# Optimization experiments

Hardware: AMD Instinct MI355X
Metric: run time of the kernel (lower is better)

The kernel has to match this reference:

```python
import jax, jax.numpy as jnp
import numpy as np

N = 100_000      # n_nodes
DEG = 32         # edge_threshold (fixed out-degree)
D = 64           # in_channels = out_channels, heads = 1
NEG_SLOPE = 0.2


def setup_inputs() -> dict:
    key = jax.random.key(0)
    k1, k2, k3, k4 = jax.random.split(key, 4)
    x = jax.random.normal(k1, (N, D), jnp.float32)
    # fixed-degree edge list with no self loops (offset in [1, N-1])
    src = jnp.repeat(jnp.arange(N, dtype=jnp.int64), DEG)
    off = jax.random.randint(k2, (N * DEG,), 1, N, dtype=jnp.int64)
    dst = (src + off) % N
    edge_index = jnp.stack([src, dst])  # [2, E]
    # glorot init as in the torch module
    stdv_w = float(np.sqrt(6.0 / (D + D)))
    weight = jax.random.uniform(k3, (D, D), jnp.float32, -stdv_w, stdv_w)
    stdv_a = float(np.sqrt(6.0 / (1 + 2 * D)))  # att is [1, heads=1, 2*D]
    att = jax.random.uniform(k4, (2 * D,), jnp.float32, -stdv_a, stdv_a)
    bias = jnp.zeros((D,), jnp.float32)
    return {"x": x, "edge_index": edge_index, "weight": weight, "att": att, "bias": bias}


def reference(x, edge_index, weight, att, bias):
    n, d = x.shape
    h = x @ weight                               # [N, D] (heads=1)
    # add self loops (inputs are constructed without self loops)
    loop = jnp.arange(n, dtype=edge_index.dtype)
    src = jnp.concatenate([edge_index[0], loop])  # message sources (x_j)
    dst = jnp.concatenate([edge_index[1], loop])  # aggregation targets (x_i)
    # GAT edge score: (cat([x_i, x_j]) * att).sum(-1) = h_i@a_i + h_j@a_j
    a_i, a_j = att[:d], att[d:]
    s_i = h @ a_i                                 # [N]
    s_j = h @ a_j                                 # [N]
    alpha = s_i[dst] + s_j[src]                   # [E+N]
    alpha = jnp.where(alpha > 0, alpha, NEG_SLOPE * alpha)  # leaky_relu
    # segment softmax over destination nodes (numerically stable)
    amax = jax.ops.segment_max(alpha, dst, num_segments=n)
    e = jnp.exp(alpha - amax[dst])
    denom = jax.ops.segment_sum(e, dst, num_segments=n)
    w = e / (denom[dst] + 1e-16)                  # [E+N]
    # weighted scatter-add aggregation of source features
    out = jax.ops.segment_sum(h[src] * w[:, None], dst, num_segments=n)  # [N, D]
    out = out + bias                              # head-mean is identity (heads=1)
    # dropout(p=0.5) is identity in eval mode; F.normalize (L2, dim=1, eps=1e-12)
    norm = jnp.linalg.norm(out, axis=1, keepdims=True)
    return out / jnp.maximum(norm, 1e-12)
```

## Files before the change

kernel.cpp:

```cpp
#include <hip/hip_runtime.h>
#include <math.h>

#define NEG_SLOPE 0.2f
#define PCHUNK 4096
#define NBINS_MAX 392
#define BIN_EDGE_CAP 8704

__device__ __forceinline__ unsigned pk_bf16x2(float a, float b) {
    unsigned ua = __float_as_uint(a);
    ua = (ua + 0x7FFFu + ((ua >> 16) & 1u)) >> 16;
    unsigned ub = __float_as_uint(b);
    ub = (ub + 0x7FFFu + ((ub >> 16) & 1u)) & 0xFFFF0000u;
    return ua | ub;
}

__global__ __launch_bounds__(256) void k_linear(const float* __restrict__ x,
        const float* __restrict__ W, const float* __restrict__ att,
        uint2* __restrict__ h16, float* __restrict__ si, float* __restrict__ sj,
        int n)
{
    int tid = threadIdx.x;
    int lane = tid & 63;
    int wv = tid >> 6;
    int q = lane >> 4;
    int f = lane & 15;

    const float4* W4 = (const float4*)W;
    float4 Wr[16];
#pragma unroll
    for (int kb = 0; kb < 16; ++kb)
        Wr[kb] = W4[(16 * q + kb) * 16 + f];

    const float4* att4 = (const float4*)att;
    float4 ai4 = att4[f];
    float4 aj4 = att4[16 + f];
    const float4* x4 = (const float4*)x;

    int row0 = (blockIdx.x * 4 + wv) * 8;
    for (int r = 0; r < 8; ++r) {
        int row = row0 + r;
        if (row >= n) break;
        size_t xb = (size_t)row * 16 + 4 * q;
        float4 xq0 = x4[xb + 0];
        float4 xq1 = x4[xb + 1];
        float4 xq2 = x4[xb + 2];
        float4 xq3 = x4[xb + 3];
        float4 acc = {0.f, 0.f, 0.f, 0.f};
#define LSTEP(xc, kb) { float4 w4 = Wr[kb]; \
        acc.x = fmaf((xc), w4.x, acc.x); acc.y = fmaf((xc), w4.y, acc.y); \
        acc.z = fmaf((xc), w4.z, acc.z); acc.w = fmaf((xc), w4.w, acc.w); }
        LSTEP(xq0.x, 0)  LSTEP(xq0.y, 1)  LSTEP(xq0.z, 2)  LSTEP(xq0.w, 3)
        LSTEP(xq1.x, 4)  LSTEP(xq1.y, 5)  LSTEP(xq1.z, 6)  LSTEP(xq1.w, 7)
        LSTEP(xq2.x, 8)  LSTEP(xq2.y, 9)  LSTEP(xq2.z, 10) LSTEP(xq2.w, 11)
        LSTEP(xq3.x, 12) LSTEP(xq3.y, 13) LSTEP(xq3.z, 14) LSTEP(xq3.w, 15)
#undef LSTEP
        acc.x += __shfl_xor(acc.x, 16); acc.x += __shfl_xor(acc.x, 32);
        acc.y += __shfl_xor(acc.y, 16); acc.y += __shfl_xor(acc.y, 32);
        acc.z += __shfl_xor(acc.z, 16); acc.z += __shfl_xor(acc.z, 32);
        acc.w += __shfl_xor(acc.w, 16); acc.w += __shfl_xor(acc.w, 32);

        if (q == 0) {
            uint2 p;
            p.x = pk_bf16x2(acc.x, acc.y);
            p.y = pk_bf16x2(acc.z, acc.w);
            h16[(size_t)row * 16 + f] = p;
        }

        float p = acc.x * ai4.x + acc.y * ai4.y + acc.z * ai4.z + acc.w * ai4.w;
        float pq = acc.x * aj4.x + acc.y * aj4.y + acc.z * aj4.z + acc.w * aj4.w;
#pragma unroll
        for (int o = 8; o >= 1; o >>= 1) {
            p += __shfl_xor(p, o);
            pq += __shfl_xor(pq, o);
        }
        if (lane == 0) { si[row] = p; sj[row] = pq; }
    }
}

__global__ __launch_bounds__(256) void k_hist(const int* __restrict__ dst, int E,
        int* __restrict__ hist_g, int NB, int nbins)
{
    __shared__ int hist[NBINS_MAX];
    int tid = threadIdx.x;
    int blk = blockIdx.x;
    int base = blk * PCHUNK;
    int cnt = E - base;
    if (cnt > PCHUNK) cnt = PCHUNK;
    for (int b = tid; b < nbins; b += 256) hist[b] = 0;
    __syncthreads();
    for (int i = tid; i < cnt; i += 256)
        atomicAdd(&hist[dst[base + i] >> 8], 1);
    __syncthreads();
    for (int b = tid; b < nbins; b += 256)
        hist_g[(size_t)b * NB + blk] = hist[b];
}

__global__ __launch_bounds__(256) void k_scan_a(int* __restrict__ data,
        int* __restrict__ bsum, int M)
{
    __shared__ int wsum[4];
    int tid = threadIdx.x;
    int lane = tid & 63;
    int wv = tid >> 6;
    int i0 = blockIdx.x * 1024 + tid * 4;
    int d0 = 0, d1 = 0, d2 = 0, d3 = 0;
    if (i0 + 3 < M) {
        int4 v = *(const int4*)(data + i0);
        d0 = v.x; d1 = v.y; d2 = v.z; d3 = v.w;
    } else {
        if (i0 + 0 < M) d0 = data[i0 + 0];
        if (i0 + 1 < M) d1 = data[i0 + 1];
        if (i0 + 2 < M) d2 = data[i0 + 2];
        if (i0 + 3 < M) d3 = data[i0 + 3];
    }
    int s = d0 + d1 + d2 + d3;
    int v = s;
#pragma unroll
    for (int o = 1; o < 64; o <<= 1) {
        int t = __shfl_up(v, o);
        if (lane >= o) v += t;
    }
    if (lane == 63) wsum[wv] = v;
    __syncthreads();
    int woff = 0;
    for (int w = 0; w < wv; ++w) woff += wsum[w];
    int ex = v - s + woff;
    if (i0 + 0 < M) data[i0 + 0] = ex; ex += d0;
    if (i0 + 1 < M) data[i0 + 1] = ex; ex += d1;
    if (i0 + 2 < M) data[i0 + 2] = ex; ex += d2;
    if (i0 + 3 < M) data[i0 + 3] = ex;
    if (tid == 255) bsum[blockIdx.x] = wsum[0] + wsum[1] + wsum[2] + wsum[3];
}

__global__ __launch_bounds__(256) void k_scan_b(const int* __restrict__ bsum,
        int* __restrict__ boff, int nb)
{
    __shared__ int wsum[4];
    int tid = threadIdx.x;
    int lane = tid & 63;
    int wv = tid >> 6;
    int t2 = tid * 2;
    int a = (t2 < nb) ? bsum[t2] : 0;
    int b = (t2 + 1 < nb) ? bsum[t2 + 1] : 0;
    int s = a + b;
    int v = s;
#pragma unroll
    for (int o = 1; o < 64; o <<= 1) {
        int t = __shfl_up(v, o);
        if (lane >= o) v += t;
    }
    if (lane == 63) wsum[wv] = v;
    __syncthreads();
    int woff = 0;
    for (int w = 0; w < wv; ++w) woff += wsum[w];
    int ex = v - s + woff;
    if (t2 < nb) boff[t2] = ex;
    if (t2 + 1 < nb) boff[t2 + 1] = ex + a;
}

__global__ __launch_bounds__(256) void k_scan_c(int* __restrict__ data,
        const int* __restrict__ boff, int M)
{
    int off = boff[blockIdx.x];
    int i0 = blockIdx.x * 1024 + threadIdx.x * 4;
#pragma unroll
    for (int k = 0; k < 4; ++k)
        if (i0 + k < M) data[i0 + k] += off;
}

__global__ __launch_bounds__(256) void k_part2(const int* __restrict__ src,
        const int* __restrict__ dst, int E,
        const int* __restrict__ hist_g, int NB, int nbins,
        unsigned* __restrict__ bin_edges)
{
    __shared__ unsigned stage[PCHUNK];
    __shared__ unsigned short sbin[PCHUNK];
    __shared__ int hist[NBINS_MAX];
    __shared__ int off[NBINS_MAX + 1];
    __shared__ int cur[NBINS_MAX];
    __shared__ int gbase[NBINS_MAX];
    __shared__ int wsum[4];

    int tid = threadIdx.x;
    int blk = blockIdx.x;
    int base = blk * PCHUNK;
    int cnt = E - base;
    if (cnt > PCHUNK) cnt = PCHUNK;

    for (int b = tid; b < nbins; b += 256) hist[b] = 0;
    __syncthreads();
    for (int i = tid; i < cnt; i += 256)
        atomicAdd(&hist[dst[base + i] >> 8], 1);
    __syncthreads();

    int lane = tid & 63;
    int wv = tid >> 6;
    int t2 = tid * 2;
    int a = (t2 < nbins) ? hist[t2] : 0;
    int b2 = (t2 + 1 < nbins) ? hist[t2 + 1] : 0;
    int s = a + b2;
    int v = s;
#pragma unroll
    for (int o = 1; o < 64; o <<= 1) {
        int t = __shfl_up(v, o);
        if (lane >= o) v += t;
    }
    if (lane == 63) wsum[wv] = v;
    __syncthreads();
    int woff = 0;
    for (int w = 0; w < wv; ++w) woff += wsum[w];
    int ex = v - s + woff;
    if (t2 <= nbins) off[t2] = ex;
    if (t2 + 1 <= nbins) off[t2 + 1] = ex + a;
    __syncthreads();

    for (int b = tid; b < nbins; b += 256) {
        cur[b] = off[b];
        gbase[b] = hist_g[(size_t)b * NB + blk];
    }
    __syncthreads();

    for (int i = tid; i < cnt; i += 256) {
        int e = base + i;
        int d = dst[e];
        int bb = d >> 8;
        int pos = atomicAdd(&cur[bb], 1);
        stage[pos] = ((unsigned)(d & 255) << 17) | (unsigned)src[e];
        sbin[pos] = (unsigned short)bb;
    }
    __syncthreads();
    for (int i = tid; i < cnt; i += 256) {
        int bb = sbin[i];
        bin_edges[gbase[bb] + (i - off[bb])] = stage[i];
    }
}

__global__ __launch_bounds__(256) void k_csr(const int* __restrict__ hist_g,
        int NB, int E, unsigned* __restrict__ bin_edges,
        int* __restrict__ row_start, int* __restrict__ deg, int n)
{
    __shared__ unsigned stage[BIN_EDGE_CAP];
    __shared__ int cnt256[256];
    __shared__ int off256[256];
    __shared__ int wsum[4];
    int b = blockIdx.x;
    int tid = threadIdx.x;
    int base = hist_g[(size_t)b * NB];
    int nxt = (b + 1 < (int)gridDim.x) ? hist_g[(size_t)(b + 1) * NB] : E;
    int cntE = nxt - base;
    if (cntE > BIN_EDGE_CAP) cntE = BIN_EDGE_CAP;

    for (int i = tid; i < cntE; i += 256) stage[i] = bin_edges[base + i];
    cnt256[tid] = 0;
    __syncthreads();
    for (int i = tid; i < cntE; i += 256)
        atomicAdd(&cnt256[stage[i] >> 17], 1);
    __syncthreads();

    int lane = tid & 63;
    int wv = tid >> 6;
    int s = cnt256[tid];
    int v = s;
#pragma unroll
    for (int o = 1; o < 64; o <<= 1) {
        int t = __shfl_up(v, o);
        if (lane >= o) v += t;
    }
    if (lane == 63) wsum[wv] = v;
    __syncthreads();
    int woff = 0;
    for (int w = 0; w < wv; ++w) woff += wsum[w];
    int ex = v - s + woff;
    off256[tid] = ex;

    int gd = b * 256 + tid;
    if (gd < n) {
        row_start[gd] = base + ex;
        deg[gd] = s;
    }
    __syncthreads();
    cnt256[tid] = ex;
    __syncthreads();
    for (int i = tid; i < cntE; i += 256) {
        unsigned pk = stage[i];
        int dl = (int)(pk >> 17);
        int pos = atomicAdd(&cnt256[dl], 1);
        bin_edges[base + pos] = pk & 0x1FFFFu;
    }
}

__global__ __launch_bounds__(256) void k_agg(const uint2* __restrict__ h16,
        const float* __restrict__ si, const float* __restrict__ sj,
        const int* __restrict__ row_start, const int* __restrict__ deg_arr,
        const unsigned* __restrict__ cols,
        const float* __restrict__ bias, float* __restrict__ out, int n)
{
    __shared__ int   sArr[4][132];
    __shared__ float wArr[4][132];
    int lane = threadIdx.x & 63;
    int wv = threadIdx.x >> 6;
    int d = blockIdx.x * 4 + wv;
    if (d >= n) return;

    int dg = deg_arr[d];
    if (dg > 128) dg = 128;
    int rs = row_start[d];
    float sid = si[d];

    int s0 = 0, s1 = 0;
    float a0 = -1e30f, a1 = -1e30f;
    if (lane < dg) {
        s0 = (int)cols[rs + lane];
        float t = sid + sj[s0];
        a0 = t > 0.f ? t : NEG_SLOPE * t;
    }
    if (lane + 64 < dg) {
        s1 = (int)cols[rs + lane + 64];
        float t = sid + sj[s1];
        a1 = t > 0.f ? t : NEG_SLOPE * t;
    }
    float tself = sid + sj[d];
    float aself = tself > 0.f ? tself : NEG_SLOPE * tself;

    float m = fmaxf(fmaxf(a0, a1), aself);
#pragma unroll
    for (int o = 32; o >= 1; o >>= 1) m = fmaxf(m, __shfl_xor(m, o));

    float e0 = (lane < dg) ? __expf(a0 - m) : 0.f;
    float e1 = (lane + 64 < dg) ? __expf(a1 - m) : 0.f;
    float eself = __expf(aself - m);

    float dsum = e0 + e1;
#pragma unroll
    for (int o = 32; o >= 1; o >>= 1) dsum += __shfl_xor(dsum, o);
    dsum += eself;

    if (lane < dg) { sArr[wv][lane] = s0; wArr[wv][lane] = e0; }
    if (lane + 64 < dg) { sArr[wv][lane + 64] = s1; wArr[wv][lane + 64] = e1; }
    if (lane == 0) { sArr[wv][dg] = d; wArr[wv][dg] = eself; }
    int cntAll = dg + 1;

    int q = lane >> 4;
    int f = lane & 15;
    float4 acc0 = {0.f, 0.f, 0.f, 0.f};
    float4 acc1 = {0.f, 0.f, 0.f, 0.f};
    int j = q;
    for (; j + 4 < cntAll; j += 8) {
        int   sA = sArr[wv][j];     float wA = wArr[wv][j];
        int   sB = sArr[wv][j + 4]; float wB = wArr[wv][j + 4];
        uint2 hA = h16[(size_t)sA * 16 + f];
        uint2 hB = h16[(size_t)sB * 16 + f];
        float ax = __uint_as_float(hA.x << 16);
        float ay = __uint_as_float(hA.x & 0xFFFF0000u);
        float az = __uint_as_float(hA.y << 16);
        float aw = __uint_as_float(hA.y & 0xFFFF0000u);
        float bx = __uint_as_float(hB.x << 16);
        float by = __uint_as_float(hB.x & 0xFFFF0000u);
        float bz = __uint_as_float(hB.y << 16);
        float bw = __uint_as_float(hB.y & 0xFFFF0000u);
        acc0.x = fmaf(wA, ax, acc0.x); acc0.y = fmaf(wA, ay, acc0.y);
        acc0.z = fmaf(wA, az, acc0.z); acc0.w = fmaf(wA, aw, acc0.w);
        acc1.x = fmaf(wB, bx, acc1.x); acc1.y = fmaf(wB, by, acc1.y);
        acc1.z = fmaf(wB, bz, acc1.z); acc1.w = fmaf(wB, bw, acc1.w);
    }
    if (j < cntAll) {
        int sA = sArr[wv][j]; float wA = wArr[wv][j];
        uint2 hA = h16[(size_t)sA * 16 + f];
        float ax = __uint_as_float(hA.x << 16);
        float ay = __uint_as_float(hA.x & 0xFFFF0000u);
        float az = __uint_as_float(hA.y << 16);
        float aw = __uint_as_float(hA.y & 0xFFFF0000u);
        acc0.x = fmaf(wA, ax, acc0.x); acc0.y = fmaf(wA, ay, acc0.y);
        acc0.z = fmaf(wA, az, acc0.z); acc0.w = fmaf(wA, aw, acc0.w);
    }
    acc0.x += acc1.x; acc0.y += acc1.y; acc0.z += acc1.z; acc0.w += acc1.w;

    acc0.x += __shfl_xor(acc0.x, 16); acc0.x += __shfl_xor(acc0.x, 32);
    acc0.y += __shfl_xor(acc0.y, 16); acc0.y += __shfl_xor(acc0.y, 32);
    acc0.z += __shfl_xor(acc0.z, 16); acc0.z += __shfl_xor(acc0.z, 32);
    acc0.w += __shfl_xor(acc0.w, 16); acc0.w += __shfl_xor(acc0.w, 32);

    float inv = 1.f / (dsum + 1e-16f);
    const float4* b4 = (const float4*)bias;
    float4 bb = b4[f];
    float4 o4;
    o4.x = acc0.x * inv + bb.x;
    o4.y = acc0.y * inv + bb.y;
    o4.z = acc0.z * inv + bb.z;
    o4.w = acc0.w * inv + bb.w;

    float nsq = o4.x * o4.x + o4.y * o4.y + o4.z * o4.z + o4.w * o4.w;
#pragma unroll
    for (int o = 8; o >= 1; o >>= 1) nsq += __shfl_xor(nsq, o);
    float rn = 1.f / fmaxf(sqrtf(nsq), 1e-12f);

    if (q == 0) {
        float4 res;
        res.x = o4.x * rn; res.y = o4.y * rn; res.z = o4.z * rn; res.w = o4.w * rn;
        ((float4*)out)[(size_t)d * 16 + f] = res;
    }
}

extern "C" void kernel_launch(void* const* d_in, const int* in_sizes, int n_in,
                              void* d_out, int out_size, void* d_ws, size_t ws_size,
                              hipStream_t stream)
{
    const float* x    = (const float*)d_in[0];
    const int*   ei   = (const int*)d_in[1];
    const float* W    = (const float*)d_in[2];
    const float* att  = (const float*)d_in[3];
    const float* bias = (const float*)d_in[4];
    float* out = (float*)d_out;

    int n = in_sizes[0] / 64;
    int E = in_sizes[1] / 2;
    const int* src = ei;
    const int* dst = ei + E;

    int nbins = (n + 255) >> 8;
    int NB = (E + PCHUNK - 1) / PCHUNK;
    int M = nbins * NB;
    int nsc = (M + 1023) / 1024;

    char* ws = (char*)d_ws;
#define CARVE(ptr, type, count) type* ptr = (type*)ws; \
        ws += (((size_t)(count) * sizeof(type)) + 255) & ~(size_t)255;
    CARVE(h16, uint2, (size_t)n * 16)
    CARVE(si, float, n)
    CARVE(sj, float, n)
    CARVE(row_start, int, n)
    CARVE(deg, int, n)
    CARVE(hist_g, int, M)
    CARVE(bsum, int, 512)
    CARVE(boff, int, 512)
    CARVE(bin_edges, unsigned, E)
#undef CARVE

    k_linear<<<(n + 31) / 32, 256, 0, stream>>>(x, W, att, h16, si, sj, n);
    k_hist<<<NB, 256, 0, stream>>>(dst, E, hist_g, NB, nbins);
    k_scan_a<<<nsc, 256, 0, stream>>>(hist_g, bsum, M);
    k_scan_b<<<1, 256, 0, stream>>>(bsum, boff, nsc);
    k_scan_c<<<nsc, 256, 0, stream>>>(hist_g, boff, M);
    k_part2<<<NB, 256, 0, stream>>>(src, dst, E, hist_g, NB, nbins, bin_edges);
    k_csr<<<nbins, 256, 0, stream>>>(hist_g, NB, E, bin_edges, row_start, deg, n);
    k_agg<<<(n + 3) / 4, 256, 0, stream>>>(h16, si, sj, row_start, deg, bin_edges, bias, out, n);
}
```

Measured before the change: 263.9 us.

## Replace binned two-pass CSR build with global atomic degree count and scatter

```diff
diff --git a/kernel.cpp b/kernel.cpp
--- a/kernel.cpp
+++ b/kernel.cpp
@@ -2,9 +2,6 @@
 #include <math.h>
 
 #define NEG_SLOPE 0.2f
-#define PCHUNK 4096
-#define NBINS_MAX 392
-#define BIN_EDGE_CAP 8704
 
 __device__ __forceinline__ unsigned pk_bf16x2(float a, float b) {
     unsigned ua = __float_as_uint(a);
@@ -17,9 +14,12 @@
 __global__ __launch_bounds__(256) void k_linear(const float* __restrict__ x,
         const float* __restrict__ W, const float* __restrict__ att,
         uint2* __restrict__ h16, float* __restrict__ si, float* __restrict__ sj,
-        int n)
+        int* __restrict__ deg, int n)
 {
     int tid = threadIdx.x;
+    int g = blockIdx.x * 256 + tid;
+    if (g < n) deg[g] = 0;
+
     int lane = tid & 63;
     int wv = tid >> 6;
     int q = lane >> 4;
@@ -77,26 +77,24 @@
     }
 }
 
-__global__ __launch_bounds__(256) void k_hist(const int* __restrict__ dst, int E,
-        int* __restrict__ hist_g, int NB, int nbins)
-{
-    __shared__ int hist[NBINS_MAX];
-    int tid = threadIdx.x;
-    int blk = blockIdx.x;
-    int base = blk * PCHUNK;
-    int cnt = E - base;
-    if (cnt > PCHUNK) cnt = PCHUNK;
-    for (int b = tid; b < nbins; b += 256) hist[b] = 0;
-    __syncthreads();
-    for (int i = tid; i < cnt; i += 256)
-        atomicAdd(&hist[dst[base + i] >> 8], 1);
-    __syncthreads();
-    for (int b = tid; b < nbins; b += 256)
-        hist_g[(size_t)b * NB + blk] = hist[b];
-}
-
-__global__ __launch_bounds__(256) void k_scan_a(int* __restrict__ data,
-        int* __restrict__ bsum, int M)
+__global__ __launch_bounds__(256) void k_deg(const int* __restrict__ dst, int E,
+        int* __restrict__ deg)
+{
+    int i = (blockIdx.x * 256 + threadIdx.x) * 4;
+    if (i + 3 < E) {
+        int4 v = *(const int4*)(dst + i);
+        atomicAdd(&deg[v.x], 1);
+        atomicAdd(&deg[v.y], 1);
+        atomicAdd(&deg[v.z], 1);
+        atomicAdd(&deg[v.w], 1);
+    } else {
+        for (int k = 0; k < 4; ++k)
+            if (i + k < E) atomicAdd(&deg[dst[i + k]], 1);
+    }
+}
+
+__global__ __launch_bounds__(256) void k_scan_a(const int* __restrict__ in,
+        int* __restrict__ out, int* __restrict__ bsum, int M)
 {
     __shared__ int wsum[4];
     int tid = threadIdx.x;
@@ -105,13 +103,13 @@
     int i0 = blockIdx.x * 1024 + tid * 4;
     int d0 = 0, d1 = 0, d2 = 0, d3 = 0;
     if (i0 + 3 < M) {
-        int4 v = *(const int4*)(data + i0);
+        int4 v = *(const int4*)(in + i0);
         d0 = v.x; d1 = v.y; d2 = v.z; d3 = v.w;
     } else {
-        if (i0 + 0 < M) d0 = data[i0 + 0];
-        if (i0 + 1 < M) d1 = data[i0 + 1];
-        if (i0 + 2 < M) d2 = data[i0 + 2];
-        if (i0 + 3 < M) d3 = data[i0 + 3];
+        if (i0 + 0 < M) d0 = in[i0 + 0];
+        if (i0 + 1 < M) d1 = in[i0 + 1];
+        if (i0 + 2 < M) d2 = in[i0 + 2];
+        if (i0 + 3 < M) d3 = in[i0 + 3];
     }
     int s = d0 + d1 + d2 + d3;
     int v = s;
@@ -125,10 +123,10 @@
     int woff = 0;
     for (int w = 0; w < wv; ++w) woff += wsum[w];
     int ex = v - s + woff;
-    if (i0 + 0 < M) data[i0 + 0] = ex; ex += d0;
-    if (i0 + 1 < M) data[i0 + 1] = ex; ex += d1;
-    if (i0 + 2 < M) data[i0 + 2] = ex; ex += d2;
-    if (i0 + 3 < M) data[i0 + 3] = ex;
+    if (i0 + 0 < M) out[i0 + 0] = ex; ex += d0;
+    if (i0 + 1 < M) out[i0 + 1] = ex; ex += d1;
+    if (i0 + 2 < M) out[i0 + 2] = ex; ex += d2;
+    if (i0 + 3 < M) out[i0 + 3] = ex;
     if (tid == 255) bsum[blockIdx.x] = wsum[0] + wsum[1] + wsum[2] + wsum[3];
 }
 
@@ -158,145 +156,52 @@
     if (t2 + 1 < nb) boff[t2 + 1] = ex + a;
 }
 
-__global__ __launch_bounds__(256) void k_scan_c(int* __restrict__ data,
-        const int* __restrict__ boff, int M)
+__global__ __launch_bounds__(256) void k_scan_c(int* __restrict__ row_start,
+        int* __restrict__ cur, const int* __restrict__ boff, int M)
 {
     int off = boff[blockIdx.x];
     int i0 = blockIdx.x * 1024 + threadIdx.x * 4;
 #pragma unroll
     for (int k = 0; k < 4; ++k)
-        if (i0 + k < M) data[i0 + k] += off;
-}
-
-__global__ __launch_bounds__(256) void k_part2(const int* __restrict__ src,
+        if (i0 + k < M) {
+            int v = row_start[i0 + k] + off;
+            row_start[i0 + k] = v;
+            cur[i0 + k] = v;
+        }
+}
+
+__global__ __launch_bounds__(256) void k_scatter(const int* __restrict__ src,
         const int* __restrict__ dst, int E,
-        const int* __restrict__ hist_g, int NB, int nbins,
-        unsigned* __restrict__ bin_edges)
-{
-    __shared__ unsigned stage[PCHUNK];
-    __shared__ unsigned short sbin[PCHUNK];
-    __shared__ int hist[NBINS_MAX];
-    __shared__ int off[NBINS_MAX + 1];
-    __shared__ int cur[NBINS_MAX];
-    __shared__ int gbase[NBINS_MAX];
-    __shared__ int wsum[4];
-
-    int tid = threadIdx.x;
-    int blk = blockIdx.x;
-    int base = blk * PCHUNK;
-    int cnt = E - base;
-    if (cnt > PCHUNK) cnt = PCHUNK;
-
-    for (int b = tid; b < nbins; b += 256) hist[b] = 0;
-    __syncthreads();
-    for (int i = tid; i < cnt; i += 256)
-        atomicAdd(&hist[dst[base + i] >> 8], 1);
-    __syncthreads();
-
-    int lane = tid & 63;
-    int wv = tid >> 6;
-    int t2 = tid * 2;
-    int a = (t2 < nbins) ? hist[t2] : 0;
-    int b2 = (t2 + 1 < nbins) ? hist[t2 + 1] : 0;
-    int s = a + b2;
-    int v = s;
-#pragma unroll
-    for (int o = 1; o < 64; o <<= 1) {
-        int t = __shfl_up(v, o);
-        if (lane >= o) v += t;
-    }
-    if (lane == 63) wsum[wv] = v;
-    __syncthreads();
-    int woff = 0;
-    for (int w = 0; w < wv; ++w) woff += wsum[w];
-    int ex = v - s + woff;
-    if (t2 <= nbins) off[t2] = ex;
-    if (t2 + 1 <= nbins) off[t2 + 1] = ex + a;
-    __syncthreads();
-
-    for (int b = tid; b < nbins; b += 256) {
-        cur[b] = off[b];
-        gbase[b] = hist_g[(size_t)b * NB + blk];
-    }
-    __syncthreads();
-
-    for (int i = tid; i < cnt; i += 256) {
-        int e = base + i;
-        int d = dst[e];
-        int bb = d >> 8;
-        int pos = atomicAdd(&cur[bb], 1);
-        stage[pos] = ((unsigned)(d & 255) << 17) | (unsigned)src[e];
-        sbin[pos] = (unsigned short)bb;
-    }
-    __syncthreads();
-    for (int i = tid; i < cnt; i += 256) {
-        int bb = sbin[i];
-        bin_edges[gbase[bb] + (i - off[bb])] = stage[i];
-    }
-}
-
-__global__ __launch_bounds__(256) void k_csr(const int* __restrict__ hist_g,
-        int NB, int E, unsigned* __restrict__ bin_edges,
-        int* __restrict__ row_start, int* __restrict__ deg, int n)
-{
-    __shared__ unsigned stage[BIN_EDGE_CAP];
-    __shared__ int cnt256[256];
-    __shared__ int off256[256];
-    __shared__ int wsum[4];
-    int b = blockIdx.x;
-    int tid = threadIdx.x;
-    int base = hist_g[(size_t)b * NB];
-    int nxt = (b + 1 < (int)gridDim.x) ? hist_g[(size_t)(b + 1) * NB] : E;
-    int cntE = nxt - base;
-    if (cntE > BIN_EDGE_CAP) cntE = BIN_EDGE_CAP;
-
-    for (int i = tid; i < cntE; i += 256) stage[i] = bin_edges[base + i];
-    cnt256[tid] = 0;
-    __syncthreads();
-    for (int i = tid; i < cntE; i += 256)
-        atomicAdd(&cnt256[stage[i] >> 17], 1);
-    __syncthreads();
-
-    int lane = tid & 63;
-    int wv = tid >> 6;
-    int s = cnt256[tid];
-    int v = s;
-#pragma unroll
-    for (int o = 1; o < 64; o <<= 1) {
-        int t = __shfl_up(v, o);
-        if (lane >= o) v += t;
-    }
-    if (lane == 63) wsum[wv] = v;
-    __syncthreads();
-    int woff = 0;
-    for (int w = 0; w < wv; ++w) woff += wsum[w];
-    int ex = v - s + woff;
-    off256[tid] = ex;
-
-    int gd = b * 256 + tid;
-    if (gd < n) {
-        row_start[gd] = base + ex;
-        deg[gd] = s;
-    }
-    __syncthreads();
-    cnt256[tid] = ex;
-    __syncthreads();
-    for (int i = tid; i < cntE; i += 256) {
-        unsigned pk = stage[i];
-        int dl = (int)(pk >> 17);
-        int pos = atomicAdd(&cnt256[dl], 1);
-        bin_edges[base + pos] = pk & 0x1FFFFu;
+        int* __restrict__ cur, int* __restrict__ cols)
+{
+    int i = (blockIdx.x * 256 + threadIdx.x) * 4;
+    if (i + 3 < E) {
+        int4 d = *(const int4*)(dst + i);
+        int4 s = *(const int4*)(src + i);
+        int p0 = atomicAdd(&cur[d.x], 1);
+        int p1 = atomicAdd(&cur[d.y], 1);
+        int p2 = atomicAdd(&cur[d.z], 1);
+        int p3 = atomicAdd(&cur[d.w], 1);
+        cols[p0] = s.x;
+        cols[p1] = s.y;
+        cols[p2] = s.z;
+        cols[p3] = s.w;
+    } else {
+        for (int k = 0; k < 4; ++k)
+            if (i + k < E) {
+                int p = atomicAdd(&cur[dst[i + k]], 1);
+                cols[p] = src[i + k];
+            }
     }
 }
 
 __global__ __launch_bounds__(256) void k_agg(const uint2* __restrict__ h16,
         const float* __restrict__ si, const float* __restrict__ sj,
         const int* __restrict__ row_start, const int* __restrict__ deg_arr,
-        const unsigned* __restrict__ cols,
+        const int* __restrict__ cols,
         const float* __restrict__ bias, float* __restrict__ out, int n)
 {
-    __shared__ int   sArr[4][132];
-    __shared__ float wArr[4][132];
+    __shared__ int2 swArr[4][132];
     int lane = threadIdx.x & 63;
     int wv = threadIdx.x >> 6;
     int d = blockIdx.x * 4 + wv;
@@ -310,12 +215,12 @@
     int s0 = 0, s1 = 0;
     float a0 = -1e30f, a1 = -1e30f;
     if (lane < dg) {
-        s0 = (int)cols[rs + lane];
+        s0 = cols[rs + lane];
         float t = sid + sj[s0];
         a0 = t > 0.f ? t : NEG_SLOPE * t;
     }
     if (lane + 64 < dg) {
-        s1 = (int)cols[rs + lane + 64];
+        s1 = cols[rs + lane + 64];
         float t = sid + sj[s1];
         a1 = t > 0.f ? t : NEG_SLOPE * t;
     }
@@ -335,45 +240,64 @@
     for (int o = 32; o >= 1; o >>= 1) dsum += __shfl_xor(dsum, o);
     dsum += eself;
 
-    if (lane < dg) { sArr[wv][lane] = s0; wArr[wv][lane] = e0; }
-    if (lane + 64 < dg) { sArr[wv][lane + 64] = s1; wArr[wv][lane + 64] = e1; }
-    if (lane == 0) { sArr[wv][dg] = d; wArr[wv][dg] = eself; }
+    if (lane < dg) swArr[wv][lane] = make_int2(s0, __float_as_int(e0));
+    if (lane + 64 < dg) swArr[wv][lane + 64] = make_int2(s1, __float_as_int(e1));
+    if (lane == 0) swArr[wv][dg] = make_int2(d, __float_as_int(eself));
     int cntAll = dg + 1;
 
     int q = lane >> 4;
     int f = lane & 15;
     float4 acc0 = {0.f, 0.f, 0.f, 0.f};
     float4 acc1 = {0.f, 0.f, 0.f, 0.f};
+    float4 acc2 = {0.f, 0.f, 0.f, 0.f};
+    float4 acc3 = {0.f, 0.f, 0.f, 0.f};
+
+#define UNPK_FMA(hv, wgt, acc) { \
+        acc.x = fmaf((wgt), __uint_as_float((hv).x << 16), acc.x); \
+        acc.y = fmaf((wgt), __uint_as_float((hv).x & 0xFFFF0000u), acc.y); \
+        acc.z = fmaf((wgt), __uint_as_float((hv).y << 16), acc.z); \
+        acc.w = fmaf((wgt), __uint_as_float((hv).y & 0xFFFF0000u), acc.w); }
+
     int j = q;
+    for (; j + 12 < cntAll; j += 16) {
+        int2 eA = swArr[wv][j];
+        int2 eB = swArr[wv][j + 4];
+        int2 eC = swArr[wv][j + 8];
+        int2 eD = swArr[wv][j + 12];
+        uint2 hA = h16[(size_t)eA.x * 16 + f];
+        uint2 hB = h16[(size_t)eB.x * 16 + f];
+        uint2 hC = h16[(size_t)eC.x * 16 + f];
+        uint2 hD = h16[(size_t)eD.x * 16 + f];
+        float wA = __int_as_float(eA.y);
+        float wB = __int_as_float(eB.y);
+        float wC = __int_as_float(eC.y);
+        float wD = __int_as_float(eD.y);
+        UNPK_FMA(hA, wA, acc0)
+        UNPK_FMA(hB, wB, acc1)
+        UNPK_FMA(hC, wC, acc2)
+        UNPK_FMA(hD, wD, acc3)
+    }
     for (; j + 4 < cntAll; j += 8) {
-        int   sA = sArr[wv][j];     float wA = wArr[wv][j];
-        int   sB = sArr[wv][j + 4]; float wB = wArr[wv][j + 4];
-        uint2 hA = h16[(size_t)sA * 16 + f];
-        uint2 hB = h16[(size_t)sB * 16 + f];
-        float ax = __uint_as_float(hA.x << 16);
-        float ay = __uint_as_float(hA.x & 0xFFFF0000u);
-        float az = __uint_as_float(hA.y << 16);
-        float aw = __uint_as_float(hA.y & 0xFFFF0000u);
-        float bx = __uint_as_float(hB.x << 16);
-        float by = __uint_as_float(hB.x & 0xFFFF0000u);
-        float bz = __uint_as_float(hB.y << 16);
-        float bw = __uint_as_float(hB.y & 0xFFFF0000u);
-        acc0.x = fmaf(wA, ax, acc0.x); acc0.y = fmaf(wA, ay, acc0.y);
-        acc0.z = fmaf(wA, az, acc0.z); acc0.w = fmaf(wA, aw, acc0.w);
-        acc1.x = fmaf(wB, bx, acc1.x); acc1.y = fmaf(wB, by, acc1.y);
-        acc1.z = fmaf(wB, bz, acc1.z); acc1.w = fmaf(wB, bw, acc1.w);
+        int2 eA = swArr[wv][j];
+        int2 eB = swArr[wv][j + 4];
+        uint2 hA = h16[(size_t)eA.x * 16 + f];
+        uint2 hB = h16[(size_t)eB.x * 16 + f];
+        float wA = __int_as_float(eA.y);
+        float wB = __int_as_float(eB.y);
+        UNPK_FMA(hA, wA, acc0)
+        UNPK_FMA(hB, wB, acc1)
     }
     if (j < cntAll) {
-        int sA = sArr[wv][j]; float wA = wArr[wv][j];
-        uint2 hA = h16[(size_t)sA * 16 + f];
-        float ax = __uint_as_float(hA.x << 16);
-        float ay = __uint_as_float(hA.x & 0xFFFF0000u);
-        float az = __uint_as_float(hA.y << 16);
-        float aw = __uint_as_float(hA.y & 0xFFFF0000u);
-        acc0.x = fmaf(wA, ax, acc0.x); acc0.y = fmaf(wA, ay, acc0.y);
-        acc0.z = fmaf(wA, az, acc0.z); acc0.w = fmaf(wA, aw, acc0.w);
-    }
+        int2 eA = swArr[wv][j];
+        uint2 hA = h16[(size_t)eA.x * 16 + f];
+        float wA = __int_as_float(eA.y);
+        UNPK_FMA(hA, wA, acc0)
+    }
+#undef UNPK_FMA
+
     acc0.x += acc1.x; acc0.y += acc1.y; acc0.z += acc1.z; acc0.w += acc1.w;
+    acc2.x += acc3.x; acc2.y += acc3.y; acc2.z += acc3.z; acc2.w += acc3.w;
+    acc0.x += acc2.x; acc0.y += acc2.y; acc0.z += acc2.z; acc0.w += acc2.w;
 
     acc0.x += __shfl_xor(acc0.x, 16); acc0.x += __shfl_xor(acc0.x, 32);
     acc0.y += __shfl_xor(acc0.y, 16); acc0.y += __shfl_xor(acc0.y, 32);
@@ -417,10 +341,8 @@
     const int* src = ei;
     const int* dst = ei + E;
 
-    int nbins = (n + 255) >> 8;
-    int NB = (E + PCHUNK - 1) / PCHUNK;
-    int M = nbins * NB;
-    int nsc = (M + 1023) / 1024;
+    int nsc = (n + 1023) / 1024;
+    int EB  = (E + 1023) / 1024;
 
     char* ws = (char*)d_ws;
 #define CARVE(ptr, type, count) type* ptr = (type*)ws; \
@@ -430,18 +352,17 @@
     CARVE(sj, float, n)
     CARVE(row_start, int, n)
     CARVE(deg, int, n)
-    CARVE(hist_g, int, M)
+    CARVE(cur, int, n)
+    CARVE(cols, int, E)
     CARVE(bsum, int, 512)
     CARVE(boff, int, 512)
-    CARVE(bin_edges, unsigned, E)
 #undef CARVE
 
-    k_linear<<<(n + 31) / 32, 256, 0, stream>>>(x, W, att, h16, si, sj, n);
-    k_hist<<<NB, 256, 0, stream>>>(dst, E, hist_g, NB, nbins);
-    k_scan_a<<<nsc, 256, 0, stream>>>(hist_g, bsum, M);
+    k_linear<<<(n + 31) / 32, 256, 0, stream>>>(x, W, att, h16, si, sj, deg, n);
+    k_deg<<<EB, 256, 0, stream>>>(dst, E, deg);
+    k_scan_a<<<nsc, 256, 0, stream>>>(deg, row_start, bsum, n);
     k_scan_b<<<1, 256, 0, stream>>>(bsum, boff, nsc);
-    k_scan_c<<<nsc, 256, 0, stream>>>(hist_g, boff, M);
-    k_part2<<<NB, 256, 0, stream>>>(src, dst, E, hist_g, NB, nbins, bin_edges);
-    k_csr<<<nbins, 256, 0, stream>>>(hist_g, NB, E, bin_edges, row_start, deg, n);
-    k_agg<<<(n + 3) / 4, 256, 0, stream>>>(h16, si, sj, row_start, deg, bin_edges, bias, out, n);
-}
+    k_scan_c<<<nsc, 256, 0, stream>>>(row_start, cur, boff, n);
+    k_scatter<<<EB, 256, 0, stream>>>(src, dst, E, cur, cols);
+    k_agg<<<(n + 3) / 4, 256, 0, stream>>>(h16, si, sj, row_start, deg, cols, bias, out, n);
+}
```

After: 626.2 us. 137% more time.
